# Performance work log

Hardware: AMD Instinct MI355X
Metric: run time of the kernel (lower is better)

Reference implementation:

```python
import jax, jax.numpy as jnp
import numpy as np

B, T, E = 32, 2048, 1024

def setup_inputs() -> dict:
    key = jax.random.key(0)
    k1, k2, k3 = jax.random.split(key, 3)
    enc = jax.random.normal(k1, (B, T, E), dtype=jnp.float32)
    ctx = jax.random.normal(k2, (B, E), dtype=jnp.float32)
    W = jax.random.normal(k3, (E, E), dtype=jnp.float32) * 0.05
    b = jnp.zeros((1, E), dtype=jnp.float32)
    return {"enc": enc, "ctx": ctx, "W": W, "b": b}

def reference(enc, ctx, W, b):
    # ht: (B, T, E) = tanh(enc @ W + b)
    ht = jnp.tanh(jnp.einsum('bte,ef->btf', enc, W) + b)
    # scores: (B, T) = batch dot of ctx against each timestep of ht
    scores = jnp.einsum('be,bte->bt', ctx, ht)
    at = jax.nn.softmax(scores, axis=-1)
    # weighted sum pooling over time -> (B, E)
    return jnp.einsum('bt,bte->be', at, ht)
```

## Files before the change

kernel.cpp:

```cpp
#include <hip/hip_runtime.h>
#include <hip/hip_bf16.h>
#include <math.h>

typedef unsigned short u16;
typedef unsigned int   u32;
typedef _Float16 f16x8 __attribute__((ext_vector_type(8)));
typedef float f32x4  __attribute__((ext_vector_type(4)));

#define Bb 32
#define Tt 2048
#define Ee 1024
#define Mm (Bb*Tt)
#define LSTR 40

__device__ __forceinline__ float tanh_fast(float x) {
  float ax = fminf(fabsf(x), 15.0f);
  float e  = __expf(2.0f * ax);
  float t  = 1.0f - 2.0f / (e + 1.0f);
  return copysignf(t, x);
}

__device__ __forceinline__ u32 pack2h(float a, float b) {
  _Float16 ha = (_Float16)a, hb = (_Float16)b;
  return (u32)__builtin_bit_cast(u16, ha) | ((u32)__builtin_bit_cast(u16, hb) << 16);
}

__global__ __launch_bounds__(256) void wt_convert(const float* __restrict__ W,
                                                  u16* __restrict__ Wt_hi,
                                                  u16* __restrict__ Wt_lo) {
  __shared__ float tile[32][33];
  int n0 = blockIdx.x * 32, k0 = blockIdx.y * 32;
  int tx = threadIdx.x, ty = threadIdx.y;
#pragma unroll
  for (int i = 0; i < 4; ++i)
    tile[ty + 8*i][tx] = W[(size_t)(k0 + ty + 8*i) * Ee + n0 + tx];
  __syncthreads();
#pragma unroll
  for (int i = 0; i < 4; ++i) {
    float v = tile[tx][ty + 8*i];
    _Float16 hi = (_Float16)v;
    float rem = v - (float)hi;
    _Float16 lo = (_Float16)rem;
    size_t idx = (size_t)(n0 + ty + 8*i) * Ee + k0 + tx;
    Wt_hi[idx] = __builtin_bit_cast(u16, hi);
    Wt_lo[idx] = __builtin_bit_cast(u16, lo);
  }
}

__global__ __launch_bounds__(256, 2) void gemm_tanh_score(
    const float* __restrict__ enc, const float* __restrict__ ctx,
    const float* __restrict__ bias,
    const u16* __restrict__ Wt_hi, const u16* __restrict__ Wt_lo,
    u16* __restrict__ ht, float* __restrict__ scores) {
  __shared__ u16 Ahf[128*LSTR], Bhi[128*LSTR], Blo[128*LSTR];

  int bx = blockIdx.x;
  int nt = bx & 7, mt = bx >> 3;
  int m0 = mt * 128, n0 = nt * 128;
  int tid = threadIdx.x;
  int w = tid >> 6, lane = tid & 63;
  int wm = (w & 1) * 64, wn = (w >> 1) * 64;
  int q = lane >> 4, c = lane & 15;

  f32x4 zero = {0.f, 0.f, 0.f, 0.f};
  f32x4 acc[4][4];
#pragma unroll
  for (int i = 0; i < 4; ++i)
#pragma unroll
    for (int j = 0; j < 4; ++j) acc[i][j] = zero;

  int ar = tid >> 1, ah = tid & 1;
  const float* Ap  = enc   + (size_t)(m0 + ar) * Ee + ah * 16;
  const u16*   BhP = Wt_hi + (size_t)(n0 + ar) * Ee + ah * 16;
  const u16*   BlP = Wt_lo + (size_t)(n0 + ar) * Ee + ah * 16;
  u16* AW  = &Ahf[ar * LSTR + ah * 16];
  u16* BhW = &Bhi[ar * LSTR + ah * 16];
  u16* BlW = &Blo[ar * LSTR + ah * 16];

  for (int kt = 0; kt < 32; ++kt) {
    const float4* ap = (const float4*)(Ap + (size_t)kt * 32);
    float4 f0 = ap[0], f1 = ap[1], f2 = ap[2], f3 = ap[3];
    const uint4* bhp = (const uint4*)(BhP + (size_t)kt * 32);
    uint4 bH0 = bhp[0], bH1 = bhp[1];
    const uint4* blp = (const uint4*)(BlP + (size_t)kt * 32);
    uint4 bL0 = blp[0], bL1 = blp[1];

    u32 a01 = pack2h(f0.x, f0.y), a23 = pack2h(f0.z, f0.w);
    u32 a45 = pack2h(f1.x, f1.y), a67 = pack2h(f1.z, f1.w);
    u32 a89 = pack2h(f2.x, f2.y), aAB = pack2h(f2.z, f2.w);
    u32 aCD = pack2h(f3.x, f3.y), aEF = pack2h(f3.z, f3.w);

    __syncthreads();
    ((uint4*)AW)[0]  = make_uint4(a01, a23, a45, a67);
    ((uint4*)AW)[1]  = make_uint4(a89, aAB, aCD, aEF);
    ((uint4*)BhW)[0] = bH0; ((uint4*)BhW)[1] = bH1;
    ((uint4*)BlW)[0] = bL0; ((uint4*)BlW)[1] = bL1;
    __syncthreads();

    f16x8 aF[4], bH[4], bL[4];
#pragma unroll
    for (int i = 0; i < 4; ++i) {
      int rax = (wm + i * 16 + c) * LSTR + q * 8;
      aF[i] = *(const f16x8*)(&Ahf[rax]);
      int rbx = (wn + i * 16 + c) * LSTR + q * 8;
      bH[i] = *(const f16x8*)(&Bhi[rbx]);
      bL[i] = *(const f16x8*)(&Blo[rbx]);
    }
#pragma unroll
    for (int i = 0; i < 4; ++i)
#pragma unroll
      for (int j = 0; j < 4; ++j) {
        acc[i][j] = __builtin_amdgcn_mfma_f32_16x16x32_f16(aF[i], bH[j], acc[i][j], 0, 0, 0);
        acc[i][j] = __builtin_amdgcn_mfma_f32_16x16x32_f16(aF[i], bL[j], acc[i][j], 0, 0, 0);
      }
  }

  int bidx = m0 >> 11;
  float ctxv[4], biasv[4];
#pragma unroll
  for (int j = 0; j < 4; ++j) {
    int col = n0 + wn + j * 16 + c;
    ctxv[j]  = ctx[bidx * Ee + col];
    biasv[j] = bias[col];
  }
#pragma unroll
  for (int i = 0; i < 4; ++i) {
#pragma unroll
    for (int r = 0; r < 4; ++r) {
      int rowG = m0 + wm + i * 16 + q * 4 + r;
      u16* hrow = ht + (size_t)rowG * Ee + n0 + wn + c;
      float s = 0.f;
#pragma unroll
      for (int j = 0; j < 4; ++j) {
        float h = tanh_fast(acc[i][j][r] + biasv[j]);
        __hip_bfloat16 hb = __float2bfloat16(h);
        hrow[j * 16] = *(u16*)&hb;
        s += h * ctxv[j];
      }
      s += __shfl_xor(s, 1); s += __shfl_xor(s, 2);
      s += __shfl_xor(s, 4); s += __shfl_xor(s, 8);
      if (c == 0) atomicAdd(&scores[rowG], s);
    }
  }
}

__global__ __launch_bounds__(256) void softmax_t(const float* __restrict__ scores,
                                                 float* __restrict__ at) {
  __shared__ float red[256];
  int b = blockIdx.x, tid = threadIdx.x;
  float v[8];
  float mx = -3.0e38f;
#pragma unroll
  for (int i = 0; i < 8; ++i) {
    v[i] = scores[b * Tt + i * 256 + tid];
    mx = fmaxf(mx, v[i]);
  }
  red[tid] = mx; __syncthreads();
  for (int s = 128; s > 0; s >>= 1) {
    if (tid < s) red[tid] = fmaxf(red[tid], red[tid + s]);
    __syncthreads();
  }
  mx = red[0]; __syncthreads();
  float sum = 0.f;
#pragma unroll
  for (int i = 0; i < 8; ++i) { v[i] = __expf(v[i] - mx); sum += v[i]; }
  red[tid] = sum; __syncthreads();
  for (int s = 128; s > 0; s >>= 1) {
    if (tid < s) red[tid] += red[tid + s];
    __syncthreads();
  }
  float inv = 1.0f / red[0];
#pragma unroll
  for (int i = 0; i < 8; ++i) at[b * Tt + i * 256 + tid] = v[i] * inv;
}

__global__ __launch_bounds__(256) void weighted_sum(const u16* __restrict__ ht,
                                                    const float* __restrict__ at,
                                                    float* __restrict__ part) {
  __shared__ float ats[64];
  int bx = blockIdx.x;
  int b = bx >> 5, tc = bx & 31;
  int tid = threadIdx.x;
  if (tid < 64) ats[tid] = at[b * Tt + tc * 64 + tid];
  __syncthreads();
  int e0 = tid * 4;
  const u16* base = ht + (size_t)(b * Tt + tc * 64) * Ee + e0;
  float s0 = 0.f, s1 = 0.f, s2 = 0.f, s3 = 0.f;
#pragma unroll 4
  for (int t = 0; t < 64; ++t) {
    float a = ats[t];
    uint2 u = *(const uint2*)(base + (size_t)t * Ee);
    s0 += a * __uint_as_float(u.x << 16);
    s1 += a * __uint_as_float(u.x & 0xffff0000u);
    s2 += a * __uint_as_float(u.y << 16);
    s3 += a * __uint_as_float(u.y & 0xffff0000u);
  }
  float4 out4 = make_float4(s0, s1, s2, s3);
  *(float4*)(part + ((size_t)(b * 32 + tc) * Ee + e0)) = out4;
}

__global__ __launch_bounds__(256) void reduce_part(const float* __restrict__ part,
                                                   float* __restrict__ out) {
  int b = blockIdx.x, tid = threadIdx.x;
  float4 s = make_float4(0.f, 0.f, 0.f, 0.f);
#pragma unroll
  for (int tc = 0; tc < 32; ++tc) {
    float4 p = ((const float4*)(part + (size_t)(b * 32 + tc) * Ee))[tid];
    s.x += p.x; s.y += p.y; s.z += p.z; s.w += p.w;
  }
  ((float4*)(out + (size_t)b * Ee))[tid] = s;
}

extern "C" void kernel_launch(void* const* d_in, const int* in_sizes, int n_in,
                              void* d_out, int out_size, void* d_ws, size_t ws_size,
                              hipStream_t stream) {
  const float* enc  = (const float*)d_in[0];
  const float* ctx  = (const float*)d_in[1];
  const float* W    = (const float*)d_in[2];
  const float* bias = (const float*)d_in[3];
  float* out = (float*)d_out;

  char* ws = (char*)d_ws;
  u16* Wt_hi = (u16*)(ws);
  u16* Wt_lo = (u16*)(ws + (size_t)2 * 1024 * 1024);
  u16* ht    = (u16*)(ws + (size_t)4 * 1024 * 1024);
  float* scores = (float*)(ws + (size_t)4 * 1024 * 1024 + (size_t)Mm * Ee * 2);
  float* at     = scores + Mm;
  float* part   = (float*)ws;

  hipMemsetAsync(scores, 0, (size_t)Mm * sizeof(float), stream);

  wt_convert<<<dim3(32, 32), dim3(32, 8), 0, stream>>>(W, Wt_hi, Wt_lo);
  gemm_tanh_score<<<dim3(4096), dim3(256), 0, stream>>>(enc, ctx, bias, Wt_hi, Wt_lo, ht, scores);
  softmax_t<<<dim3(32), dim3(256), 0, stream>>>(scores, at);
  weighted_sum<<<dim3(1024), dim3(256), 0, stream>>>(ht, at, part);
  reduce_part<<<dim3(32), dim3(256), 0, stream>>>(part, out);
}
```

Baseline: 713.0 us.

## Double-buffer GEMM LDS tiles with direct global-to-LDS loads and XOR swizzle

Rewrites the main GEMM loop to double-buffer the A and B tiles in shared memory. The next tile is prefetched while MFMAs run on the current one, which leaves a single barrier per iteration. B tiles are loaded straight into LDS with global_load_lds, and an XOR swizzle replaces the padded stride to avoid bank conflicts. It also remaps block indices so each XCD handles a contiguous M range for L2 locality, raises the occupancy target to 3 blocks per CU, and sets wave priority around the MFMA section. The costs are more LDS per block, register pressure under launch_bounds 3, and reliance on correct swizzle and async-load ordering.

```diff
diff --git a/kernel.cpp b/kernel.cpp
--- a/kernel.cpp
+++ b/kernel.cpp
@@ -11,7 +11,6 @@
 #define Tt 2048
 #define Ee 1024
 #define Mm (Bb*Tt)
-#define LSTR 40
 
 __device__ __forceinline__ float tanh_fast(float x) {
   float ax = fminf(fabsf(x), 15.0f);
@@ -23,6 +22,12 @@
 __device__ __forceinline__ u32 pack2h(float a, float b) {
   _Float16 ha = (_Float16)a, hb = (_Float16)b;
   return (u32)__builtin_bit_cast(u16, ha) | ((u32)__builtin_bit_cast(u16, hb) << 16);
+}
+
+__device__ __forceinline__ void glds16(const u16* g, u16* l) {
+  __builtin_amdgcn_global_load_lds(
+      (const __attribute__((address_space(1))) void*)g,
+      (__attribute__((address_space(3))) void*)l, 16, 0, 0);
 }
 
 __global__ __launch_bounds__(256) void wt_convert(const float* __restrict__ W,
@@ -47,20 +52,26 @@
   }
 }
 
-__global__ __launch_bounds__(256, 2) void gemm_tanh_score(
+__global__ __launch_bounds__(256, 3) void gemm_tanh_score(
     const float* __restrict__ enc, const float* __restrict__ ctx,
     const float* __restrict__ bias,
     const u16* __restrict__ Wt_hi, const u16* __restrict__ Wt_lo,
     u16* __restrict__ ht, float* __restrict__ scores) {
-  __shared__ u16 Ahf[128*LSTR], Bhi[128*LSTR], Blo[128*LSTR];
+  __shared__ __align__(16) u16 Ah[2*4096];
+  __shared__ __align__(16) u16 BhS[2*4096];
+  __shared__ __align__(16) u16 BlS[2*4096];
 
   int bx = blockIdx.x;
-  int nt = bx & 7, mt = bx >> 3;
+  int xcd = bx & 7, lb = bx >> 3;
+  int nt = lb & 7, mtl = lb >> 3;
+  int mt = xcd * 64 + mtl;
   int m0 = mt * 128, n0 = nt * 128;
+
   int tid = threadIdx.x;
   int w = tid >> 6, lane = tid & 63;
   int wm = (w & 1) * 64, wn = (w >> 1) * 64;
   int q = lane >> 4, c = lane & 15;
+  int fch = (q ^ ((c >> 1) & 3)) * 8;
 
   f32x4 zero = {0.f, 0.f, 0.f, 0.f};
   f32x4 acc[4][4];
@@ -70,49 +81,79 @@
     for (int j = 0; j < 4; ++j) acc[i][j] = zero;
 
   int ar = tid >> 1, ah = tid & 1;
-  const float* Ap  = enc   + (size_t)(m0 + ar) * Ee + ah * 16;
-  const u16*   BhP = Wt_hi + (size_t)(n0 + ar) * Ee + ah * 16;
-  const u16*   BlP = Wt_lo + (size_t)(n0 + ar) * Ee + ah * 16;
-  u16* AW  = &Ahf[ar * LSTR + ah * 16];
-  u16* BhW = &Bhi[ar * LSTR + ah * 16];
-  u16* BlW = &Blo[ar * LSTR + ah * 16];
-
+  const float4* Abase = (const float4*)(enc + (size_t)(m0 + ar) * Ee + ah * 16);
+  int awr = ar * 32;
+  int asw = (ar >> 1) & 3;
+  int ac0 = ((2*ah + 0) ^ asw) * 8;
+  int ac1 = ((2*ah + 1) ^ asw) * 8;
+
+  int cidx0 = w * 2, cidx1 = w * 2 + 1;
+  int r0 = cidx0 * 16 + (lane >> 2);
+  int r1 = cidx1 * 16 + (lane >> 2);
+  int lg0 = ((lane & 3) ^ ((r0 >> 1) & 3)) * 8;
+  int lg1 = ((lane & 3) ^ ((r1 >> 1) & 3)) * 8;
+  const u16* Bh0 = Wt_hi + (size_t)(n0 + r0) * Ee + lg0;
+  const u16* Bh1 = Wt_hi + (size_t)(n0 + r1) * Ee + lg1;
+  const u16* Bl0 = Wt_lo + (size_t)(n0 + r0) * Ee + lg0;
+  const u16* Bl1 = Wt_lo + (size_t)(n0 + r1) * Ee + lg1;
+  int bws0 = cidx0 * 512, bws1 = cidx1 * 512;
+
+  {
+    float4 f0 = Abase[0], f1 = Abase[1], f2 = Abase[2], f3 = Abase[3];
+    glds16(Bh0, &BhS[bws0]);
+    glds16(Bh1, &BhS[bws1]);
+    glds16(Bl0, &BlS[bws0]);
+    glds16(Bl1, &BlS[bws1]);
+    u32 p0 = pack2h(f0.x, f0.y), p1 = pack2h(f0.z, f0.w);
+    u32 p2 = pack2h(f1.x, f1.y), p3 = pack2h(f1.z, f1.w);
+    u32 p4 = pack2h(f2.x, f2.y), p5 = pack2h(f2.z, f2.w);
+    u32 p6 = pack2h(f3.x, f3.y), p7 = pack2h(f3.z, f3.w);
+    *(uint4*)&Ah[awr + ac0] = make_uint4(p0, p1, p2, p3);
+    *(uint4*)&Ah[awr + ac1] = make_uint4(p4, p5, p6, p7);
+    __syncthreads();
+  }
+
+#pragma unroll 2
   for (int kt = 0; kt < 32; ++kt) {
-    const float4* ap = (const float4*)(Ap + (size_t)kt * 32);
-    float4 f0 = ap[0], f1 = ap[1], f2 = ap[2], f3 = ap[3];
-    const uint4* bhp = (const uint4*)(BhP + (size_t)kt * 32);
-    uint4 bH0 = bhp[0], bH1 = bhp[1];
-    const uint4* blp = (const uint4*)(BlP + (size_t)kt * 32);
-    uint4 bL0 = blp[0], bL1 = blp[1];
-
-    u32 a01 = pack2h(f0.x, f0.y), a23 = pack2h(f0.z, f0.w);
-    u32 a45 = pack2h(f1.x, f1.y), a67 = pack2h(f1.z, f1.w);
-    u32 a89 = pack2h(f2.x, f2.y), aAB = pack2h(f2.z, f2.w);
-    u32 aCD = pack2h(f3.x, f3.y), aEF = pack2h(f3.z, f3.w);
-
-    __syncthreads();
-    ((uint4*)AW)[0]  = make_uint4(a01, a23, a45, a67);
-    ((uint4*)AW)[1]  = make_uint4(a89, aAB, aCD, aEF);
-    ((uint4*)BhW)[0] = bH0; ((uint4*)BhW)[1] = bH1;
-    ((uint4*)BlW)[0] = bL0; ((uint4*)BlW)[1] = bL1;
-    __syncthreads();
-
-    f16x8 aF[4], bH[4], bL[4];
-#pragma unroll
-    for (int i = 0; i < 4; ++i) {
-      int rax = (wm + i * 16 + c) * LSTR + q * 8;
-      aF[i] = *(const f16x8*)(&Ahf[rax]);
-      int rbx = (wn + i * 16 + c) * LSTR + q * 8;
-      bH[i] = *(const f16x8*)(&Bhi[rbx]);
-      bL[i] = *(const f16x8*)(&Blo[rbx]);
-    }
+    int cur = (kt & 1) * 4096, nxt = 4096 - cur;
+    float4 f0, f1, f2, f3;
+    if (kt < 31) {
+      const float4* ap = Abase + (size_t)(kt + 1) * 8;
+      f0 = ap[0]; f1 = ap[1]; f2 = ap[2]; f3 = ap[3];
+      size_t ko = (size_t)(kt + 1) * 32;
+      glds16(Bh0 + ko, &BhS[nxt + bws0]);
+      glds16(Bh1 + ko, &BhS[nxt + bws1]);
+      glds16(Bl0 + ko, &BlS[nxt + bws0]);
+      glds16(Bl1 + ko, &BlS[nxt + bws1]);
+    }
+
+    f16x8 aF[4];
 #pragma unroll
     for (int i = 0; i < 4; ++i)
-#pragma unroll
-      for (int j = 0; j < 4; ++j) {
-        acc[i][j] = __builtin_amdgcn_mfma_f32_16x16x32_f16(aF[i], bH[j], acc[i][j], 0, 0, 0);
-        acc[i][j] = __builtin_amdgcn_mfma_f32_16x16x32_f16(aF[i], bL[j], acc[i][j], 0, 0, 0);
+      aF[i] = *(const f16x8*)&Ah[cur + (wm + i*16 + c) * 32 + fch];
+
+    __builtin_amdgcn_s_setprio(1);
+#pragma unroll
+    for (int j = 0; j < 4; ++j) {
+      f16x8 bH = *(const f16x8*)&BhS[cur + (wn + j*16 + c) * 32 + fch];
+      f16x8 bL = *(const f16x8*)&BlS[cur + (wn + j*16 + c) * 32 + fch];
+#pragma unroll
+      for (int i = 0; i < 4; ++i) {
+        acc[i][j] = __builtin_amdgcn_mfma_f32_16x16x32_f16(aF[i], bH, acc[i][j], 0, 0, 0);
+        acc[i][j] = __builtin_amdgcn_mfma_f32_16x16x32_f16(aF[i], bL, acc[i][j], 0, 0, 0);
       }
+    }
+    __builtin_amdgcn_s_setprio(0);
+
+    if (kt < 31) {
+      u32 p0 = pack2h(f0.x, f0.y), p1 = pack2h(f0.z, f0.w);
+      u32 p2 = pack2h(f1.x, f1.y), p3 = pack2h(f1.z, f1.w);
+      u32 p4 = pack2h(f2.x, f2.y), p5 = pack2h(f2.z, f2.w);
+      u32 p6 = pack2h(f3.x, f3.y), p7 = pack2h(f3.z, f3.w);
+      *(uint4*)&Ah[nxt + awr + ac0] = make_uint4(p0, p1, p2, p3);
+      *(uint4*)&Ah[nxt + awr + ac1] = make_uint4(p4, p5, p6, p7);
+    }
+    __syncthreads();
   }
 
   int bidx = m0 >> 11;
```

Result: faster. 690.0 us (-3.2%).
